# Optimization experiments

Hardware: AMD Instinct MI355X
Metric: run time of the kernel (lower is better)

Reference implementation:

```python
import jax, jax.numpy as jnp
import numpy as np

N_NODES = 50000
N_EDGES = 800000
N_GRAPHS = 64
PERIOD = 10
HID = 300
NLAYER = 5
EPS = 1e-5


def setup_inputs() -> dict:
    key = jax.random.key(0)
    ks = jax.random.split(key, 16)
    batch = jnp.sort(jax.random.randint(ks[0], (N_NODES,), 0, N_GRAPHS))
    x = jax.random.normal(ks[1], (N_NODES, 2 * PERIOD), dtype=jnp.float32)
    edge_index = jax.random.randint(ks[2], (2, N_EDGES), 0, N_NODES)
    edge_attr = jax.random.normal(ks[3], (N_EDGES,), dtype=jnp.float32)

    def xavier(k, fan_in, fan_out, shape):
        a = float(np.sqrt(6.0 / (fan_in + fan_out)))
        return jax.random.uniform(k, shape, jnp.float32, -a, a)

    linW = xavier(ks[4], 2 * PERIOD, HID, (2 * PERIOD, HID))
    linb = jnp.zeros((HID,), jnp.float32)
    W1s = xavier(ks[5], HID, 2 * HID, (NLAYER, HID, 2 * HID))
    b1s = jnp.zeros((NLAYER, 2 * HID), jnp.float32)
    g1s = jnp.ones((NLAYER, 2 * HID), jnp.float32)
    be1s = jnp.zeros((NLAYER, 2 * HID), jnp.float32)
    W2s = xavier(ks[6], 2 * HID, HID, (NLAYER, 2 * HID, HID))
    b2s = jnp.zeros((NLAYER, HID), jnp.float32)
    gos = jnp.ones((NLAYER, HID), jnp.float32)
    bos = jnp.zeros((NLAYER, HID), jnp.float32)
    return {"batch": batch, "x": x, "edge_index": edge_index, "edge_attr": edge_attr,
            "linW": linW, "linb": linb, "W1s": W1s, "b1s": b1s, "g1s": g1s,
            "be1s": be1s, "W2s": W2s, "b2s": b2s, "gos": gos, "bos": bos}


def _bn(h, g, b):
    # training-mode BatchNorm1d: batch mean, biased variance
    m = jnp.mean(h, axis=0)
    v = jnp.var(h, axis=0)
    return g * (h - m) * jax.lax.rsqrt(v + EPS) + b


def reference(batch, x, edge_index, edge_attr, linW, linb, W1s, b1s, g1s, be1s, W2s, b2s, gos, bos):
    src, dst = edge_index[0], edge_index[1]
    ew = edge_attr[:, None]  # [E,1]
    h = x @ linW + linb  # [N, HID]
    for i in range(NLAYER):
        # gather-modulate-scatter message passing (sign=False: message = w * x_j)
        msg = ew * h[src]  # [E, HID]
        agg = jax.ops.segment_sum(msg, dst, num_segments=N_NODES)  # [N, HID]
        # inner MLP with BatchNorm
        t = agg @ W1s[i] + b1s[i]  # [N, 2*HID]
        t = jax.nn.relu(_bn(t, g1s[i], be1s[i]))
        t = t @ W2s[i] + b2s[i]  # [N, HID]
        # outer BatchNorm
        h = _bn(t, gos[i], bos[i])
        if i != NLAYER - 1:
            h = jax.nn.relu(h)
    xpool = jax.ops.segment_sum(h, batch, num_segments=N_GRAPHS)  # [G, HID]
    return (h, xpool)
```

## Files before the change

### kernel.cpp

```cpp
#include <hip/hip_runtime.h>
#include <hip/hip_fp16.h>
#include <stdint.h>

typedef _Float16 f16x8 __attribute__((ext_vector_type(8)));
typedef unsigned short u16x8 __attribute__((ext_vector_type(8)));
typedef float f32x4 __attribute__((ext_vector_type(4)));

constexpr int NN  = 50000;
constexpr int NE  = 800000;
constexpr int NG  = 64;
constexpr int H   = 300;
constexpr int H2  = 600;
constexpr int IND = 20;
constexpr int NL  = 5;

constexpr int MP  = 50048;
constexpr int KP1 = 320;
constexpr int KP2 = 608;
constexpr int NP1 = 640;
constexpr int NP2 = 384;
constexpr int HCS = 320;

constexpr int SCAN_B = (NN + 1023) / 1024;

static __device__ __forceinline__ ushort f2h(float f) {
  return __half_as_ushort(__float2half(f));
}
static __device__ __forceinline__ float h2f_lo(uint32_t u) {
  return __half2float(__ushort_as_half((ushort)(u & 0xFFFFu)));
}
static __device__ __forceinline__ float h2f_hi(uint32_t u) {
  return __half2float(__ushort_as_half((ushort)(u >> 16)));
}
static __device__ __forceinline__ uint32_t packh(float a, float b) {
  return (uint32_t)f2h(a) | ((uint32_t)f2h(b) << 16);
}

static __device__ __forceinline__ f16x8 relu8(f16x8 t) {
#if __has_builtin(__builtin_elementwise_max)
  f16x8 z = 0;
  return __builtin_elementwise_max(t, z);
#else
  u16x8 u = *reinterpret_cast<u16x8*>(&t);
  u = u & (u16x8)((u >> 15) - (unsigned short)1);
  return *reinterpret_cast<f16x8*>(&u);
#endif
}


__global__ void hist_kernel(const int* __restrict__ dst, int* __restrict__ hist) {
  int i = blockIdx.x * blockDim.x + threadIdx.x;
  if (i < NE) atomicAdd(&hist[dst[i]], 1);
}

__global__ __launch_bounds__(1024) void scan1_kernel(const int* __restrict__ hist,
                                                     int* __restrict__ offs,
                                                     int* __restrict__ bsum) {
  __shared__ int sdata[1024];
  int b = blockIdx.x, tid = threadIdx.x;
  int i = b * 1024 + tid;
  int v = (i < NN) ? hist[i] : 0;
  sdata[tid] = v;
  __syncthreads();
  for (int ofs = 1; ofs < 1024; ofs <<= 1) {
    int t = (tid >= ofs) ? sdata[tid - ofs] : 0;
    __syncthreads();
    sdata[tid] += t;
    __syncthreads();
  }
  if (i < NN) offs[i] = sdata[tid] - v;
  if (tid == 1023) bsum[b] = sdata[1023];
}

__global__ void scan2_kernel(const int* __restrict__ bsum, int* __restrict__ bpre) {
  if (threadIdx.x == 0) {
    int run = 0;
    for (int b = 0; b < SCAN_B; ++b) {
      bpre[b] = run;
      run += bsum[b];
    }
    bpre[SCAN_B] = run;
  }
}

__global__ __launch_bounds__(1024) void scan3_kernel(const int* __restrict__ bpre,
                                                     int* __restrict__ offs,
                                                     int* __restrict__ cursor) {
  int b = blockIdx.x, tid = threadIdx.x;
  int i = b * 1024 + tid;
  if (i < NN) {
    int o = offs[i] + bpre[b];
    offs[i] = o;
    cursor[i] = o;
  }
  if (i == 0) offs[NN] = bpre[SCAN_B];
}

__global__ void scatter_kernel(const int* __restrict__ src, const int* __restrict__ dst,
                               const float* __restrict__ w, int* __restrict__ cursor,
                               int* __restrict__ ssrc, float* __restrict__ sw) {
  int i = blockIdx.x * blockDim.x + threadIdx.x;
  if (i < NE) {
    int d = dst[i];
    int p = atomicAdd(&cursor[d], 1);
    ssrc[p] = src[i];
    sw[p]   = w[i];
  }
}


__global__ void padzero_kernel(ushort* __restrict__ b, int KPAD, int Ntrue) {
  long long nA = (long long)(MP - NN) * KPAD;
  int padc = KPAD - Ntrue;
  long long nB = (long long)NN * padc;
  long long total = nA + nB;
  long long stride = (long long)gridDim.x * blockDim.x;
  for (long long i = blockIdx.x * (long long)blockDim.x + threadIdx.x; i < total; i += stride) {
    long long off;
    if (i < nA) {
      off = (long long)NN * KPAD + i;
    } else {
      long long j = i - nA;
      long long r = j / padc;
      long long c = Ntrue + (j - r * padc);
      off = r * KPAD + c;
    }
    b[off] = 0;
  }
}


__global__ void packW1_kernel(const float* __restrict__ W1s, ushort* __restrict__ Wp) {
  int idx = blockIdx.x * blockDim.x + threadIdx.x;
  if (idx >= NL * NP1 * KP1) return;
  int i = idx / (NP1 * KP1);
  int rem = idx - i * (NP1 * KP1);
  int n = rem / KP1;
  int k = rem - n * KP1;
  float v = (n < H2 && k < H) ? W1s[((long long)i * H + k) * H2 + n] : 0.f;
  Wp[idx] = f2h(v);
}

__global__ void packW2_kernel(const float* __restrict__ W2s, ushort* __restrict__ Wp) {
  int idx = blockIdx.x * blockDim.x + threadIdx.x;
  if (idx >= NL * NP2 * KP2) return;
  int i = idx / (NP2 * KP2);
  int rem = idx - i * (NP2 * KP2);
  int n = rem / KP2;
  int k = rem - n * KP2;
  float v = (n < H && k < H2) ? W2s[((long long)i * H2 + k) * H + n] : 0.f;
  Wp[idx] = f2h(v);
}


__global__ __launch_bounds__(256) void lin_kernel(const float* __restrict__ x,
                                                  const float* __restrict__ W,
                                                  const float* __restrict__ b,
                                                  ushort* __restrict__ hc) {
  __shared__ float Ws[IND * H];
  __shared__ float bs[H];
  int tid = threadIdx.x;
  for (int i = tid; i < IND * H; i += 256) Ws[i] = W[i];
  for (int i = tid; i < H; i += 256) bs[i] = b[i];
  __syncthreads();
  const int QPR = H / 4;
  int total = NN * QPR;
  for (int idx = blockIdx.x * 256 + tid; idx < total; idx += gridDim.x * 256) {
    int n = idx / QPR;
    int f = (idx - n * QPR) * 4;
    float a0 = bs[f], a1 = bs[f + 1], a2 = bs[f + 2], a3 = bs[f + 3];
    const float* xr = x + n * IND;
#pragma unroll
    for (int k = 0; k < IND; ++k) {
      float xv = xr[k];
      const float* wk = &Ws[k * H + f];
      a0 = fmaf(xv, wk[0], a0);
      a1 = fmaf(xv, wk[1], a1);
      a2 = fmaf(xv, wk[2], a2);
      a3 = fmaf(xv, wk[3], a3);
    }
    uint2 o = make_uint2(packh(a0, a1), packh(a2, a3));
    *reinterpret_cast<uint2*>(hc + (long long)n * HCS + f) = o;
  }
}


__global__ __launch_bounds__(192) void agg_kernel(const ushort* __restrict__ hc,
                                                  const int* __restrict__ offs,
                                                  const int* __restrict__ ssrc,
                                                  const float* __restrict__ sw,
                                                  ushort* __restrict__ agg) {
  int n = blockIdx.x;
  int t = threadIdx.x;
  if (t >= H / 2) return;
  int s = offs[n], e = offs[n + 1];
  float a0 = 0.f, a1 = 0.f;
  int i = s;
  for (; i + 7 < e; i += 8) {
    uint32_t u[8];
    float w[8];
#pragma unroll
    for (int j = 0; j < 8; ++j) {
      int sn = ssrc[i + j];
      w[j] = sw[i + j];
      u[j] = *reinterpret_cast<const uint32_t*>(hc + (long long)sn * HCS + 2 * t);
    }
#pragma unroll
    for (int j = 0; j < 8; ++j) {
      a0 = fmaf(w[j], h2f_lo(u[j]), a0);
      a1 = fmaf(w[j], h2f_hi(u[j]), a1);
    }
  }
  for (; i < e; ++i) {
    int sn = ssrc[i];
    float w = sw[i];
    uint32_t u = *reinterpret_cast<const uint32_t*>(hc + (long long)sn * HCS + 2 * t);
    a0 = fmaf(w, h2f_lo(u), a0);
    a1 = fmaf(w, h2f_hi(u), a1);
  }
  *reinterpret_cast<uint32_t*>(agg + (long long)n * KP1 + 2 * t) = packh(a0, a1);
}


template <bool FUSE_BN>
__global__ __launch_bounds__(64, 4) void gemm_mfma(
    const ushort* __restrict__ A, const ushort* __restrict__ Bp,
    const float* __restrict__ bias, ushort* __restrict__ C,
    float* __restrict__ sum, float* __restrict__ sq,
    int M, int Ntrue, int Ktiles, int KPAD, int Cstride, int ntiles,
    const ushort* __restrict__ bns, const ushort* __restrict__ bnh) {
  __shared__ ushort AL[2][64 * 32];
  int nwg = gridDim.x;
  int hw = blockIdx.x;
  int xcd = hw & 7, slot = hw >> 3;
  int q = nwg >> 3, r = nwg & 7;
  int logical = (xcd < r ? xcd * (q + 1) : r * (q + 1) + (xcd - r) * q) + slot;
  int mt = logical / ntiles;
  int nt = logical - mt * ntiles;

  int lane = threadIdx.x & 63;
  int lm = lane & 15, lg = lane >> 4;
  long long bm = (long long)mt * 64;
  long long bn = (long long)nt * 64;

  int srow = lane >> 2;
  int slotc = lane & 3;

  const ushort* Bb = Bp + (bn + lm) * KPAD + lg * 8;

  f32x4 acc[4][4] = {};

  auto stageA = [&](int buf, int kt) {
    int k0 = kt * 32;
#pragma unroll
    for (int j = 0; j < 4; ++j) {
      int row = j * 16 + srow;
      int cg = slotc ^ ((row >> 1) & 3);
      long long go = (bm + row) * KPAD + k0 + cg * 8;
      ushort* l = &AL[buf][(j * 16) * 32];
      __builtin_amdgcn_global_load_lds(
          (const __attribute__((address_space(1))) void*)(A + go),
          (__attribute__((address_space(3))) void*)l, 16, 0, 0);
    }
  };

  stageA(0, 0);

  for (int kt = 0; kt < Ktiles; ++kt) {
    int cur = kt & 1;
    int nk = kt + 1;
    f16x8 b[4];
#pragma unroll
    for (int i = 0; i < 4; ++i)
      b[i] = *reinterpret_cast<const f16x8*>(Bb + (long long)i * 16 * KPAD + kt * 32);
    if (nk < Ktiles) {
      stageA(nk & 1, nk);
      asm volatile("s_waitcnt vmcnt(4)" ::: "memory");
    } else {
      asm volatile("s_waitcnt vmcnt(0)" ::: "memory");
    }
    f16x8 a[4];
#pragma unroll
    for (int i = 0; i < 4; ++i) {
      int row = i * 16 + lm;
      int c = lg ^ ((row >> 1) & 3);
      a[i] = *reinterpret_cast<const f16x8*>(&AL[cur][row * 32 + c * 8]);
    }
    if constexpr (FUSE_BN) {
      int kbase = kt * 32 + lg * 8;
      f16x8 sv = *reinterpret_cast<const f16x8*>(bns + kbase);
      f16x8 hv = *reinterpret_cast<const f16x8*>(bnh + kbase);
#pragma unroll
      for (int i = 0; i < 4; ++i) a[i] = relu8(a[i] * sv + hv);
    }
#pragma unroll
    for (int mf = 0; mf < 4; ++mf)
#pragma unroll
      for (int nf = 0; nf < 4; ++nf)
        acc[mf][nf] = __builtin_amdgcn_mfma_f32_16x16x32_f16(a[mf], b[nf], acc[mf][nf], 0, 0, 0);
  }

  int colb = (int)bn + lm;
#pragma unroll
  for (int nf = 0; nf < 4; ++nf) {
    int col = colb + nf * 16;
    bool cok = col < Ntrue;
    float bv = cok ? bias[col] : 0.f;
    float cs = 0.f, cq = 0.f;
#pragma unroll
    for (int mf = 0; mf < 4; ++mf) {
      int row0 = (int)bm + mf * 16 + lg * 4;
      f32x4 v = acc[mf][nf];
#pragma unroll
      for (int e = 0; e < 4; ++e) {
        float w = v[e] + bv;
        bool ok = cok && (row0 + e < M);
        if (ok) {
          cs += w;
          cq = fmaf(w, w, cq);
        }
        float wp = __shfl_xor(w, 1);
        if (ok && ((lm & 1) == 0)) {
          *reinterpret_cast<uint32_t*>(&C[(long long)(row0 + e) * Cstride + col]) = packh(w, wp);
        }
      }
    }
    cs += __shfl_xor(cs, 16);
    cq += __shfl_xor(cq, 16);
    cs += __shfl_xor(cs, 32);
    cq += __shfl_xor(cq, 32);
    if (lg == 0 && cok) {
      atomicAdd(&sum[col], cs);
      atomicAdd(&sq[col], cq);
    }
  }
}


__global__ void finalize_kernel(const float* __restrict__ sum, const float* __restrict__ sq,
                                const float* __restrict__ g, const float* __restrict__ be,
                                int C, int Calloc, float invM, float* __restrict__ scale,
                                float* __restrict__ shift, ushort* __restrict__ scaleh,
                                ushort* __restrict__ shifth) {
  int c = blockIdx.x * blockDim.x + threadIdx.x;
  if (c >= Calloc) return;
  float sc = 0.f, sh = 0.f;
  if (c < C) {
    float m = sum[c] * invM;
    float v = sq[c] * invM - m * m;
    sc = g[c] * rsqrtf(v + 1e-5f);
    sh = be[c] - m * sc;
  }
  scale[c] = sc;
  shift[c] = sh;
  if (scaleh) {
    scaleh[c] = f2h(sc);
    shifth[c] = f2h(sh);
  }
}

template <bool LAST>
__global__ void bn2_kernel(const ushort* __restrict__ u_, const float* __restrict__ scale,
                           const float* __restrict__ shift, ushort* __restrict__ hc,
                           float* __restrict__ out) {
  const int QPR = H / 4;
  int total = NN * QPR;
  for (int idx = blockIdx.x * blockDim.x + threadIdx.x; idx < total;
       idx += gridDim.x * blockDim.x) {
    int r = idx / QPR;
    int c = (idx - r * QPR) * 4;
    uint2 u = *reinterpret_cast<const uint2*>(u_ + (long long)r * KP1 + c);
    float4 sc = *reinterpret_cast<const float4*>(scale + c);
    float4 sh = *reinterpret_cast<const float4*>(shift + c);
    float w0 = fmaf(h2f_lo(u.x), sc.x, sh.x);
    float w1 = fmaf(h2f_hi(u.x), sc.y, sh.y);
    float w2 = fmaf(h2f_lo(u.y), sc.z, sh.z);
    float w3 = fmaf(h2f_hi(u.y), sc.w, sh.w);
    if (LAST) {
      *reinterpret_cast<float4*>(out + (long long)r * H + c) = make_float4(w0, w1, w2, w3);
    } else {
      w0 = fmaxf(w0, 0.f);
      w1 = fmaxf(w1, 0.f);
      w2 = fmaxf(w2, 0.f);
      w3 = fmaxf(w3, 0.f);
      *reinterpret_cast<uint2*>(hc + (long long)r * HCS + c) =
          make_uint2(packh(w0, w1), packh(w2, w3));
    }
  }
}


__global__ void bounds_kernel(const int* __restrict__ batch, int* __restrict__ gstart) {
  int g = threadIdx.x;
  if (g > NG) return;
  if (g == NG) { gstart[NG] = NN; return; }
  int lo = 0, hi = NN;
  while (lo < hi) {
    int mid = (lo + hi) >> 1;
    if (batch[mid] < g) lo = mid + 1; else hi = mid;
  }
  gstart[g] = lo;
}

__global__ __launch_bounds__(320) void pool_kernel(const float* __restrict__ h,
                                                   const int* __restrict__ gstart,
                                                   float* __restrict__ xpool) {
  int g = blockIdx.x;
  int f = threadIdx.x;
  if (f >= H) return;
  int s = gstart[g], e = gstart[g + 1];
  float acc = 0.f;
  for (int r = s + blockIdx.y; r < e; r += gridDim.y) acc += h[(long long)r * H + f];
  atomicAdd(&xpool[g * H + f], acc);
}


extern "C" void kernel_launch(void* const* d_in, const int* in_sizes, int n_in,
                              void* d_out, int out_size, void* d_ws, size_t ws_size,
                              hipStream_t stream) {
  const int*   batch = (const int*)d_in[0];
  const float* x     = (const float*)d_in[1];
  const int*   eidx  = (const int*)d_in[2];
  const float* eattr = (const float*)d_in[3];
  const float* linW  = (const float*)d_in[4];
  const float* linb  = (const float*)d_in[5];
  const float* W1s   = (const float*)d_in[6];
  const float* b1s   = (const float*)d_in[7];
  const float* g1s   = (const float*)d_in[8];
  const float* be1s  = (const float*)d_in[9];
  const float* W2s   = (const float*)d_in[10];
  const float* b2s   = (const float*)d_in[11];
  const float* gos   = (const float*)d_in[12];
  const float* bos   = (const float*)d_in[13];

  const int* esrc = eidx;
  const int* edst = eidx + NE;

  char* p = (char*)d_ws;
  auto alloc = [&](size_t bytes) {
    char* r = p;
    p += (bytes + 255) & ~(size_t)255;
    return r;
  };
  ushort* tb   = (ushort*)alloc((size_t)MP * KP2 * 2);
  ushort* ub   = (ushort*)alloc((size_t)MP * KP1 * 2);
  ushort* hc   = (ushort*)alloc((size_t)NN * HCS * 2);
  ushort* W1p  = (ushort*)alloc((size_t)NL * NP1 * KP1 * 2);
  ushort* W2p  = (ushort*)alloc((size_t)NL * NP2 * KP2 * 2);
  int*    hist   = (int*)alloc((size_t)NN * 4);
  int*    offs   = (int*)alloc((size_t)(NN + 64) * 4);
  int*    cursor = (int*)alloc((size_t)NN * 4);
  int*    ssrc   = (int*)alloc((size_t)NE * 4);
  float*  sw     = (float*)alloc((size_t)NE * 4);
  int*    bsum   = (int*)alloc((size_t)(SCAN_B + 1) * 4);
  int*    bpre   = (int*)alloc((size_t)(SCAN_B + 1) * 4);
  float*  sum1   = (float*)alloc((size_t)(H2 * 2 + H * 2) * 4);
  float*  sq1    = sum1 + H2;
  float*  sum2   = sq1 + H2;
  float*  sq2    = sum2 + H;
  float*  scale1 = (float*)alloc((size_t)(KP2 * 2 + H * 2) * 4);
  float*  shift1 = scale1 + KP2;
  float*  scale2 = shift1 + KP2;
  float*  shift2 = scale2 + H;
  ushort* scaleh = (ushort*)alloc((size_t)KP2 * 2 * 2);
  ushort* shifth = scaleh + KP2;
  int*    gstart = (int*)alloc((size_t)(NG + 1) * 4);
  size_t needed = (size_t)(p - (char*)d_ws);
  if (ws_size < needed) return;

  float* hout  = (float*)d_out;
  float* xpool = hout + (long long)NN * H;

  padzero_kernel<<<1024, 256, 0, stream>>>(tb, KP2, H2);
  padzero_kernel<<<1024, 256, 0, stream>>>(ub, KP1, H);

  packW1_kernel<<<(NL * NP1 * KP1 + 255) / 256, 256, 0, stream>>>(W1s, W1p);
  packW2_kernel<<<(NL * NP2 * KP2 + 255) / 256, 256, 0, stream>>>(W2s, W2p);

  hipMemsetAsync(hist, 0, (size_t)NN * 4, stream);
  hist_kernel<<<(NE + 255) / 256, 256, 0, stream>>>(edst, hist);
  scan1_kernel<<<SCAN_B, 1024, 0, stream>>>(hist, offs, bsum);
  scan2_kernel<<<1, 64, 0, stream>>>(bsum, bpre);
  scan3_kernel<<<SCAN_B, 1024, 0, stream>>>(bpre, offs, cursor);
  scatter_kernel<<<(NE + 255) / 256, 256, 0, stream>>>(esrc, edst, eattr, cursor, ssrc, sw);

  lin_kernel<<<4096, 256, 0, stream>>>(x, linW, linb, hc);

  const int MT = MP / 64;
  for (int i = 0; i < NL; ++i) {
    agg_kernel<<<NN, 192, 0, stream>>>(hc, offs, ssrc, sw, ub);
    hipMemsetAsync(sum1, 0, (size_t)(H2 * 2 + H * 2) * 4, stream);

    gemm_mfma<false><<<MT * (NP1 / 64), 64, 0, stream>>>(
        ub, W1p + (size_t)i * NP1 * KP1, b1s + (size_t)i * H2, tb,
        sum1, sq1, NN, H2, KP1 / 32, KP1, KP2, NP1 / 64, nullptr, nullptr);
    finalize_kernel<<<(KP2 + 255) / 256, 256, 0, stream>>>(
        sum1, sq1, g1s + (size_t)i * H2, be1s + (size_t)i * H2, H2, KP2, 1.f / NN,
        scale1, shift1, scaleh, shifth);

    gemm_mfma<true><<<MT * (NP2 / 64), 64, 0, stream>>>(
        tb, W2p + (size_t)i * NP2 * KP2, b2s + (size_t)i * H, ub,
        sum2, sq2, NN, H, KP2 / 32, KP2, KP1, NP2 / 64, scaleh, shifth);
    finalize_kernel<<<(H + 255) / 256, 256, 0, stream>>>(
        sum2, sq2, gos + (size_t)i * H, bos + (size_t)i * H, H, H, 1.f / NN,
        scale2, shift2, nullptr, nullptr);
    if (i < NL - 1) {
      bn2_kernel<false><<<4096, 256, 0, stream>>>(ub, scale2, shift2, hc, hout);
    } else {
      bn2_kernel<true><<<4096, 256, 0, stream>>>(ub, scale2, shift2, hc, hout);
    }
  }

  hipMemsetAsync(xpool, 0, (size_t)NG * H * 4, stream);
  bounds_kernel<<<1, 128, 0, stream>>>(batch, gstart);
  pool_kernel<<<dim3(NG, 8), 320, 0, stream>>>(hout, gstart, xpool);
}
```

Before: 1.377 ms.

## Load GEMM A tiles directly into registers with register double-buffering

```diff
diff --git a/kernel.cpp b/kernel.cpp
--- a/kernel.cpp
+++ b/kernel.cpp
@@ -223,13 +223,12 @@
 
 
 template <bool FUSE_BN>
-__global__ __launch_bounds__(64, 4) void gemm_mfma(
+__global__ __launch_bounds__(64, 3) void gemm_mfma(
     const ushort* __restrict__ A, const ushort* __restrict__ Bp,
     const float* __restrict__ bias, ushort* __restrict__ C,
     float* __restrict__ sum, float* __restrict__ sq,
     int M, int Ntrue, int Ktiles, int KPAD, int Cstride, int ntiles,
     const ushort* __restrict__ bns, const ushort* __restrict__ bnh) {
-  __shared__ ushort AL[2][64 * 32];
   int nwg = gridDim.x;
   int hw = blockIdx.x;
   int xcd = hw & 7, slot = hw >> 3;
@@ -243,49 +242,30 @@
   long long bm = (long long)mt * 64;
   long long bn = (long long)nt * 64;
 
-  int srow = lane >> 2;
-  int slotc = lane & 3;
-
+  const ushort* Ab = A + (bm + lm) * KPAD + lg * 8;
   const ushort* Bb = Bp + (bn + lm) * KPAD + lg * 8;
 
   f32x4 acc[4][4] = {};
-
-  auto stageA = [&](int buf, int kt) {
-    int k0 = kt * 32;
-#pragma unroll
-    for (int j = 0; j < 4; ++j) {
-      int row = j * 16 + srow;
-      int cg = slotc ^ ((row >> 1) & 3);
-      long long go = (bm + row) * KPAD + k0 + cg * 8;
-      ushort* l = &AL[buf][(j * 16) * 32];
-      __builtin_amdgcn_global_load_lds(
-          (const __attribute__((address_space(1))) void*)(A + go),
-          (__attribute__((address_space(3))) void*)l, 16, 0, 0);
-    }
-  };
-
-  stageA(0, 0);
+  f16x8 aC[4], aN[4], bC[4], bN[4];
+
+#pragma unroll
+  for (int i = 0; i < 4; ++i) {
+    aC[i] = *reinterpret_cast<const f16x8*>(Ab + (long long)i * 16 * KPAD);
+    bC[i] = *reinterpret_cast<const f16x8*>(Bb + (long long)i * 16 * KPAD);
+  }
 
   for (int kt = 0; kt < Ktiles; ++kt) {
-    int cur = kt & 1;
     int nk = kt + 1;
-    f16x8 b[4];
-#pragma unroll
-    for (int i = 0; i < 4; ++i)
-      b[i] = *reinterpret_cast<const f16x8*>(Bb + (long long)i * 16 * KPAD + kt * 32);
     if (nk < Ktiles) {
-      stageA(nk & 1, nk);
-      asm volatile("s_waitcnt vmcnt(4)" ::: "memory");
-    } else {
-      asm volatile("s_waitcnt vmcnt(0)" ::: "memory");
+#pragma unroll
+      for (int i = 0; i < 4; ++i) {
+        aN[i] = *reinterpret_cast<const f16x8*>(Ab + (long long)i * 16 * KPAD + nk * 32);
+        bN[i] = *reinterpret_cast<const f16x8*>(Bb + (long long)i * 16 * KPAD + nk * 32);
+      }
     }
     f16x8 a[4];
 #pragma unroll
-    for (int i = 0; i < 4; ++i) {
-      int row = i * 16 + lm;
-      int c = lg ^ ((row >> 1) & 3);
-      a[i] = *reinterpret_cast<const f16x8*>(&AL[cur][row * 32 + c * 8]);
-    }
+    for (int i = 0; i < 4; ++i) a[i] = aC[i];
     if constexpr (FUSE_BN) {
       int kbase = kt * 32 + lg * 8;
       f16x8 sv = *reinterpret_cast<const f16x8*>(bns + kbase);
@@ -297,7 +277,12 @@
     for (int mf = 0; mf < 4; ++mf)
 #pragma unroll
       for (int nf = 0; nf < 4; ++nf)
-        acc[mf][nf] = __builtin_amdgcn_mfma_f32_16x16x32_f16(a[mf], b[nf], acc[mf][nf], 0, 0, 0);
+        acc[mf][nf] = __builtin_amdgcn_mfma_f32_16x16x32_f16(a[mf], bC[nf], acc[mf][nf], 0, 0, 0);
+#pragma unroll
+    for (int i = 0; i < 4; ++i) {
+      aC[i] = aN[i];
+      bC[i] = bN[i];
+    }
   }
 
   int colb = (int)bn + lm;
```

Result: slower. 1.492 ms (+8.3%).
